# Kernel tuning notes

Measured on AMD Instinct MI355X. Metric: run time of the kernel, lower is better.

Reference implementation:

```python
import jax, jax.numpy as jnp
from jax import lax
import numpy as np
import math

B, LBL, PRED, CIN = 16, 48, 336, 7
L = LBL + PRED
DM, E = 512, 2
DIN, N, DCONV = 2 * DM, 16, 4
DTR = math.ceil(DM / 16)  # 32
TF = 4  # freq='h' time features
EPS = 1e-5


def _ln(x, w, b):
    m = x.mean(-1, keepdims=True)
    v = ((x - m) ** 2).mean(-1, keepdims=True)
    return (x - m) / jnp.sqrt(v + EPS) * w + b


def _silu(x):
    return x * jax.nn.sigmoid(x)


def _token_embed(x, w):
    # Conv1d(c_in, d_model, k=3, padding=1, circular, bias=False). x: (B,L,C), w: (DM,C,3)
    xp = jnp.concatenate([x[:, -1:], x, x[:, :1]], axis=1)  # circular pad along L
    y = lax.conv_general_dilated(xp.transpose(0, 2, 1), w, (1,), 'VALID',
                                 dimension_numbers=('NCH', 'OIH', 'NCH'))
    return y.transpose(0, 2, 1)  # (B,L,DM)


def _selective_scan(u, dt, A, Bm, Cm):
    # u,dt: (B,L,DIN); A: (DIN,N); Bm,Cm: (B,L,N)
    h0 = jnp.zeros((u.shape[0], DIN, N), u.dtype)

    def step(h, inp):
        u_t, dt_t, B_t, C_t = inp  # (B,DIN),(B,DIN),(B,N),(B,N)
        dA = jnp.exp(dt_t[:, :, None] * A)  # (B,DIN,N)
        h = dA * h + (dt_t * u_t)[:, :, None] * B_t[:, None, :]
        y = jnp.einsum('bdn,bn->bd', h, C_t)
        return h, y

    _, ys = lax.scan(step, h0, (u.transpose(1, 0, 2), dt.transpose(1, 0, 2),
                                Bm.transpose(1, 0, 2), Cm.transpose(1, 0, 2)))
    return ys.transpose(1, 0, 2)  # (B,L,DIN)


def _mamba(x, p):
    (in_w, conv_w, conv_b, xproj_w, dtproj_w, dtproj_b, A_log, Dp, out_w) = p
    xz = x @ in_w.T                      # (B,L,2*DIN)
    xin, z = jnp.split(xz, 2, axis=-1)
    # depthwise causal conv1d, kernel DCONV
    xt = jnp.pad(xin.transpose(0, 2, 1), ((0, 0), (0, 0), (DCONV - 1, 0)))
    xc = lax.conv_general_dilated(xt, conv_w, (1,), 'VALID', feature_group_count=DIN,
                                  dimension_numbers=('NCH', 'OIH', 'NCH'))
    xc = _silu((xc + conv_b[None, :, None]).transpose(0, 2, 1))  # (B,L,DIN)
    dbc = xc @ xproj_w.T                 # (B,L,DTR+2N)
    dt_r, Bm, Cm = dbc[..., :DTR], dbc[..., DTR:DTR + N], dbc[..., DTR + N:]
    dt = jax.nn.softplus(dt_r @ dtproj_w.T + dtproj_b)  # (B,L,DIN)
    A = -jnp.exp(A_log)                  # (DIN,N)
    y = _selective_scan(xc, dt, A, Bm, Cm) + xc * Dp
    y = y * _silu(z)
    return y @ out_w.T                   # (B,L,DM)


def _model(x_dec, x_mark_dec, token_w, timef_w, layer_ps, fin_w, fin_b, out_w):
    mean = lax.stop_gradient(x_dec[:, :LBL].mean(1, keepdims=True))
    head = x_dec[:, :LBL] - mean
    std = lax.stop_gradient(jnp.sqrt(head.var(axis=1, keepdims=True) + EPS))
    head = head / std
    xd = jnp.concatenate([head, x_dec[:, LBL:]], axis=1)
    x = _token_embed(xd, token_w) + x_mark_dec @ timef_w.T  # DataEmbedding_wo_pos (eval: no dropout)
    for i in range(E):
        nw, nb = layer_ps[0][i], layer_ps[1][i]
        mp = tuple(layer_ps[j][i] for j in range(2, 11))
        x = x + _mamba(_ln(x, nw, nb), mp)
    x = _ln(x, fin_w, fin_b)
    out = x @ out_w.T
    out = out * std + mean
    return out[:, -PRED:, :]


def setup_inputs() -> dict:
    key = jax.random.key(0)
    ks = jax.random.split(key, 20)
    s = 0.02
    d = {
        'x_enc': jax.random.normal(ks[0], (B, 96, CIN), jnp.float32),
        'x_mark_enc': jax.random.normal(ks[1], (B, 96, TF), jnp.float32),
        'x_dec': jax.random.normal(ks[2], (B, L, CIN), jnp.float32),
        'x_mark_dec': jax.random.normal(ks[3], (B, L, TF), jnp.float32),
        'token_w': jax.random.normal(ks[4], (DM, CIN, 3), jnp.float32) * s,
        'timef_w': jax.random.normal(ks[5], (DM, TF), jnp.float32) * s,
        'norm_w': jnp.ones((E, DM), jnp.float32),
        'norm_b': jnp.zeros((E, DM), jnp.float32),
        'in_proj_w': jax.random.normal(ks[6], (E, 2 * DIN, DM), jnp.float32) * s,
        'conv_w': jax.random.normal(ks[7], (E, DIN, 1, DCONV), jnp.float32) * s,
        'conv_b': jnp.zeros((E, DIN), jnp.float32),
        'xproj_w': jax.random.normal(ks[8], (E, DTR + 2 * N, DIN), jnp.float32) * s,
        'dtproj_w': jax.random.normal(ks[9], (E, DIN, DTR), jnp.float32) * s,
        'dtproj_b': jnp.full((E, DIN), -4.0, jnp.float32),
        'A_log': jnp.tile(jnp.log(jnp.arange(1, N + 1, dtype=jnp.float32)), (E, DIN, 1)),
        'D': jnp.ones((E, DIN), jnp.float32),
        'outproj_w': jax.random.normal(ks[10], (E, DM, DIN), jnp.float32) * s,
        'final_norm_w': jnp.ones((DM,), jnp.float32),
        'final_norm_b': jnp.zeros((DM,), jnp.float32),
        'out_w': jax.random.normal(ks[11], (CIN, DM), jnp.float32) * s,
    }
    return d


def reference(x_enc, x_mark_enc, x_dec, x_mark_dec, token_w, timef_w, norm_w, norm_b,
              in_proj_w, conv_w, conv_b, xproj_w, dtproj_w, dtproj_b, A_log, D,
              outproj_w, final_norm_w, final_norm_b, out_w):
    layer_ps = (norm_w, norm_b, in_proj_w, conv_w, conv_b, xproj_w, dtproj_w,
                dtproj_b, A_log, D, outproj_w)
    return _model(x_dec, x_mark_dec, token_w, timef_w, layer_ps,
                  final_norm_w, final_norm_b, out_w)
```

## Files before the change

kernel.cpp:

```cpp
#include <hip/hip_runtime.h>

#define B_    16
#define LBL_  48
#define PRED_ 336
#define CIN_  7
#define L_    384
#define DM_   512
#define E_    2
#define DIN_  1024
#define N_    16
#define DCONV_ 4
#define DTR_  32
#define TF_   4
#define EPSF  1e-5f
#define NSEG  16
#define SEGL  24
#define SC2   2
#define NCHK  12

typedef unsigned short u16;
typedef __attribute__((ext_vector_type(8))) short short8;
typedef __attribute__((ext_vector_type(4))) float f32x4;

__device__ __forceinline__ float bf2f(u16 u){
  union { float f; unsigned int i; } cv; cv.i = ((unsigned int)u) << 16; return cv.f;
}
__device__ __forceinline__ u16 f2bf(float f){
  union { float f; unsigned int i; } cv; cv.f = f;
  unsigned int x = cv.i;
  unsigned int lsb = (x >> 16) & 1u;
  x += 0x7fffu + lsb;
  return (u16)(x >> 16);
}
__device__ __forceinline__ float lo16(unsigned int v){
  union { float f; unsigned int i; } cv; cv.i = v << 16; return cv.f;
}
__device__ __forceinline__ float hi16(unsigned int v){
  union { float f; unsigned int i; } cv; cv.i = v & 0xffff0000u; return cv.f;
}

#define GLDS(g, l) __builtin_amdgcn_global_load_lds( \
    (const __attribute__((address_space(1))) void*)(g), \
    (__attribute__((address_space(3))) void*)(l), 16, 0, 0)

#define PO_XDEC   0
#define PO_XMARK  43008
#define PO_TOKW   67584
#define PO_TIMEF  78336
#define PO_NORMW  80384
#define PO_NORMB  81408
#define PO_INW    82432
#define PO_CONVW  2179584
#define PO_CONVB  2187776
#define PO_XPROJ  2189824
#define PO_DTW    2320896
#define PO_DTB    2386432
#define PO_ALOG   2388480
#define PO_DP     2421248
#define PO_OUTW   2423296
#define PO_FNW    3471872
#define PO_FNB    3472384
#define PO_HEADW  3472896
#define P_TOTAL   3476480
#define A_X    3476480
#define A_LNB  6622208
#define A_XZ   9767936
#define A_DT   22350848
#define A_DBC  28642304
#define A_MEAN 29078528
#define A_STD  29078640
#define A_DBC4 16059392
#define DBC_SL ((size_t)(B_*L_)*64)
#define A_XCB_OFF 3145728

struct Ptrs { const void* p[18]; };

__device__ __forceinline__ float wredsum(float s){
  #pragma unroll
  for (int off = 32; off; off >>= 1) s += __shfl_xor(s, off, 64);
  return s;
}

__device__ __forceinline__ void qpowers(float q, float* p){
  float q2 = q*q;
  float q4 = q2*q2;
  float q8 = q4*q4;
  float q3 = q2*q;
  p[0]=q;      p[1]=q2;     p[2]=q3;     p[3]=q4;
  p[4]=q4*q;   p[5]=q4*q2;  p[6]=q4*q3;  p[7]=q8;
  p[8]=q8*q;   p[9]=q8*q2;  p[10]=q8*q3; p[11]=q8*q4;
  p[12]=q8*p[4]; p[13]=q8*p[5]; p[14]=q8*p[6]; p[15]=q8*q8;
}

__device__ __forceinline__ unsigned int xcd_swz(unsigned int bid, unsigned int nwg){
  return (bid & 7u) * (nwg >> 3) + (bid >> 3);
}

__global__ __launch_bounds__(256) void convert_kernel(Ptrs ps, float* __restrict__ dst){
  const int offs[18] = {PO_XDEC, PO_XMARK, PO_TOKW, PO_TIMEF, PO_NORMW, PO_NORMB,
                        PO_INW, PO_CONVW, PO_CONVB, PO_XPROJ, PO_DTW, PO_DTB,
                        PO_ALOG, PO_DP, PO_OUTW, PO_FNW, PO_FNB, PO_HEADW};
  int idx = blockIdx.x * 256 + threadIdx.x;
  if (idx >= P_TOTAL) return;
  int seg = 0;
  #pragma unroll
  for (int s = 1; s < 18; s++) if (idx >= offs[s]) seg = s;
  int off = idx - offs[seg];
  int isbf = (((const u16*)ps.p[4])[0] == 0x3F80u);
  if (seg == 6 || seg == 9 || seg == 10 || seg == 14){
    u16 hv = isbf ? ((const u16*)ps.p[seg])[off]
                  : f2bf(((const float*)ps.p[seg])[off]);
    ((u16*)(dst + offs[seg]))[off] = hv;
  } else {
    float v = isbf ? bf2f(((const u16*)ps.p[seg])[off])
                   : ((const float*)ps.p[seg])[off];
    dst[idx] = v;
  }
}

__global__ __launch_bounds__(256) void embed_ln_kernel(const float* __restrict__ x_dec,
      const float* __restrict__ token_w, const float* __restrict__ x_mark,
      const float* __restrict__ timef_w, const float* __restrict__ nw,
      const float* __restrict__ nb, float* __restrict__ x, u16* __restrict__ out,
      float* __restrict__ meanv, float* __restrict__ stdv){
  __shared__ float sm[8], siv[8], ssd[8];
  int wv = threadIdx.x >> 6;
  int lane = threadIdx.x & 63;
  int tok = blockIdx.x*4 + wv;
  int t = tok % L_;
  int b = tok / L_;
  for (int c = wv; c < CIN_; c += 4){
    float v0 = (lane < LBL_) ? x_dec[(b*L_+lane)*CIN_+c] : 0.f;
    float m = wredsum(v0) * (1.f/LBL_);
    float dv = (lane < LBL_) ? (v0 - m) : 0.f;
    float sd = sqrtf(wredsum(dv*dv) * (1.f/LBL_) + EPSF);
    if (lane == 0){ sm[c] = m; siv[c] = 1.f/sd; ssd[c] = sd; }
  }
  __syncthreads();
  if ((blockIdx.x % (L_/4)) == 0 && threadIdx.x < CIN_){
    meanv[b*CIN_ + threadIdx.x] = sm[threadIdx.x];
    stdv[b*CIN_ + threadIdx.x]  = ssd[threadIdx.x];
  }
  int tm1 = (t == 0) ? L_-1 : t-1;
  int tp1 = (t == L_-1) ? 0 : t+1;
  auto ldx = [&](int row, int c){
    float v = x_dec[(b*L_+row)*CIN_+c];
    return (row < LBL_) ? (v - sm[c]) * siv[c] : v;
  };
  const float* mk = x_mark + (b*L_+t)*TF_;
  float a0[CIN_], a1[CIN_], a2[CIN_], mkv[TF_];
  #pragma unroll
  for (int ci = 0; ci < CIN_; ci++){ a0[ci]=ldx(tm1,ci); a1[ci]=ldx(t,ci); a2[ci]=ldx(tp1,ci); }
  #pragma unroll
  for (int f = 0; f < TF_; f++) mkv[f] = mk[f];
  float v[8];
  #pragma unroll
  for (int j = 0; j < 8; j++){
    int d = lane*8 + j;
    float acc = 0.f;
    #pragma unroll
    for (int ci = 0; ci < CIN_; ci++){
      const float* w = token_w + (d*CIN_+ci)*3;
      acc += a0[ci]*w[0] + a1[ci]*w[1] + a2[ci]*w[2];
    }
    #pragma unroll
    for (int f = 0; f < TF_; f++)
      acc += mkv[f] * timef_w[d*TF_+f];
    v[j] = acc;
  }
  float* xr = x + (size_t)tok*DM_ + lane*8;
  *(float4*)xr       = (float4){v[0],v[1],v[2],v[3]};
  *(float4*)(xr + 4) = (float4){v[4],v[5],v[6],v[7]};
  float s = (v[0]+v[1])+(v[2]+v[3])+((v[4]+v[5])+(v[6]+v[7]));
  float mean = wredsum(s) * (1.f/DM_);
  float s2 = 0.f;
  #pragma unroll
  for (int j = 0; j < 8; j++){ v[j] -= mean; s2 += v[j]*v[j]; }
  float rstd = rsqrtf(wredsum(s2) * (1.f/DM_) + EPSF);
  const float* wr = nw + lane*8;
  const float* br = nb + lane*8;
  uint4 o; unsigned int* op = (unsigned int*)&o;
  #pragma unroll
  for (int k = 0; k < 4; k++){
    u16 e0 = f2bf(v[2*k]   * rstd * wr[2*k]   + br[2*k]);
    u16 e1 = f2bf(v[2*k+1] * rstd * wr[2*k+1] + br[2*k+1]);
    op[k] = (unsigned int)e0 | ((unsigned int)e1 << 16);
  }
  *(uint4*)(out + (size_t)tok*DM_ + lane*8) = o;
}

__global__ __launch_bounds__(256) void ln_kernel(const float* __restrict__ x,
     const float* __restrict__ w, const float* __restrict__ bias, u16* __restrict__ out){
  int tok = blockIdx.x*4 + (threadIdx.x >> 6);
  int lane = threadIdx.x & 63;
  const float* xr = x + (size_t)tok*DM_ + lane*8;
  float4 a = *(const float4*)xr;
  float4 bq = *(const float4*)(xr + 4);
  float v[8] = {a.x,a.y,a.z,a.w,bq.x,bq.y,bq.z,bq.w};
  float s = (v[0]+v[1])+(v[2]+v[3])+((v[4]+v[5])+(v[6]+v[7]));
  float mean = wredsum(s) * (1.f/DM_);
  float s2 = 0.f;
  #pragma unroll
  for (int j = 0; j < 8; j++){ v[j] -= mean; s2 += v[j]*v[j]; }
  float rstd = rsqrtf(wredsum(s2) * (1.f/DM_) + EPSF);
  const float* wr = w + lane*8;
  const float* br = bias + lane*8;
  uint4 o; unsigned int* op = (unsigned int*)&o;
  #pragma unroll
  for (int k = 0; k < 4; k++){
    u16 e0 = f2bf(v[2*k]   * rstd * wr[2*k]   + br[2*k]);
    u16 e1 = f2bf(v[2*k+1] * rstd * wr[2*k+1] + br[2*k+1]);
    op[k] = (unsigned int)e0 | ((unsigned int)e1 << 16);
  }
  *(uint4*)(out + (size_t)tok*DM_ + lane*8) = o;
}

__global__ __launch_bounds__(256) void inproj_conv(const u16* __restrict__ A,
    const u16* __restrict__ Wt, const float* __restrict__ cw, const float* __restrict__ cb,
    u16* __restrict__ xz, u16* __restrict__ xcb){
  __shared__ u16 As[384 * 64];
  __shared__ u16 Ws[64 * 64];
  int tid = threadIdx.x;
  int wv = tid >> 6, lane = tid & 63;
  unsigned int bid = blockIdx.y * 32 + blockIdx.x;
  unsigned int swz = xcd_swz(bid, 512);
  int b  = (int)(swz >> 5);
  int n0 = (int)(swz & 31) * 64;
  int m0 = b * L_;
  int la = lane & 15, lk = lane >> 4;
  f32x4 acc[6][4];
  #pragma unroll
  for (int i = 0; i < 6; i++)
    #pragma unroll
    for (int j = 0; j < 4; j++) acc[i][j] = (f32x4){0.f,0.f,0.f,0.f};
  int sr = lane >> 3;
  int sc = (((lane & 7) ^ (sr & 7)) * 8);
  const u16* Ag = A + (size_t)(m0 + wv*96 + sr) * DM_ + sc;
  u16* Al = As + (wv*96)*64 + lane*8;
  const u16* Wg = Wt + (size_t)(n0 + wv*16 + sr) * DM_ + sc;
  u16* Wl = Ws + (wv*16)*64 + lane*8;
  for (int k0 = 0; k0 < DM_; k0 += 64){
    #pragma unroll
    for (int i = 0; i < 12; i++) GLDS(Ag + (size_t)(i*8)*DM_ + k0, Al + i*512);
    #pragma unroll
    for (int i = 0; i < 2; i++)  GLDS(Wg + (size_t)(i*8)*DM_ + k0, Wl + i*512);
    __syncthreads();
    #pragma unroll
    for (int ks = 0; ks < 2; ks++){
      int ch = (ks*4 + lk) ^ (la & 7);
      short8 af[6], bfr[4];
      #pragma unroll
      for (int mi = 0; mi < 6; mi++) af[mi] = *(const short8*)&As[(wv*96 + mi*16 + la)*64 + ch*8];
      #pragma unroll
      for (int ni = 0; ni < 4; ni++) bfr[ni] = *(const short8*)&Ws[(ni*16 + la)*64 + ch*8];
      #pragma unroll
      for (int mi = 0; mi < 6; mi++)
        #pragma unroll
        for (int ni = 0; ni < 4; ni++)
          acc[mi][ni] = __builtin_amdgcn_mfma_f32_16x16x32_bf16(af[mi], bfr[ni], acc[mi][ni], 0, 0, 0);
    }
    __syncthreads();
  }
  #pragma unroll
  for (int mi = 0; mi < 6; mi++)
    #pragma unroll
    for (int ni = 0; ni < 4; ni++){
      int colc = ni*2 + (la >> 3);
      #pragma unroll
      for (int r = 0; r < 4; r++){
        int row = wv*96 + mi*16 + lk*4 + r;
        As[row*64 + ((colc ^ (row & 7))<<3) + (la & 7)] = f2bf(acc[mi][ni][r]);
      }
    }
  __syncthreads();
  int c8 = (tid & 7) * 8;
  int tg = tid >> 3;
  if (n0 < DIN_){
    float4 w[8]; float bias[8];
    #pragma unroll
    for (int k = 0; k < 8; k++){
      w[k] = *(const float4*)(cw + (n0 + c8 + k)*4);
      bias[k] = cb[n0 + c8 + k];
    }
    for (int i = 0; i < 12; i++){
      int t = tg*12 + i;
      uint4 tap[4];
      #pragma unroll
      for (int j = 0; j < 4; j++){
        int rr = t - 3 + j;
        if (rr >= 0)
          tap[j] = *(const uint4*)&As[rr*64 + ((((c8>>3) ^ (rr & 7)))<<3)];
      }
      float v[8];
      #pragma unroll
      for (int k = 0; k < 8; k++){
        float s = bias[k];
        #pragma unroll
        for (int j = 0; j < 4; j++){
          if (j >= 3 - t){
            const unsigned int* tp = (const unsigned int*)&tap[j];
            float xv = (k & 1) ? hi16(tp[k >> 1]) : lo16(tp[k >> 1]);
            s += xv * ((const float*)&w[k])[j];
          }
        }
        v[k] = s / (1.f + __expf(-s));
      }
      uint4 o; unsigned int* op = (unsigned int*)&o;
      #pragma unroll
      for (int k = 0; k < 4; k++)
        op[k] = (unsigned int)f2bf(v[2*k]) | ((unsigned int)f2bf(v[2*k+1]) << 16);
      *(uint4*)(xcb + (size_t)(m0 + t)*DIN_ + n0 + c8) = o;
    }
  } else {
    for (int i = 0; i < 12; i++){
      int t = tg*12 + i;
      uint4 vq = *(const uint4*)&As[t*64 + ((((c8>>3) ^ (t & 7)))<<3)];
      *(uint4*)(xz + (size_t)(m0 + t)*(2*DIN_) + n0 + c8) = vq;
    }
  }
}

template<int TN, int ACCUM, int BF16OUT>
__global__ __launch_bounds__(256) void gemm_mfma(const u16* __restrict__ A, const u16* __restrict__ Wt,
    void* __restrict__ C, int M, int N, int K){
  constexpr int WN = TN / 2;
  constexpr int NI = WN / 16;
  __shared__ u16 As[128 * 64];
  __shared__ u16 Ws[TN * 64];
  int tid = threadIdx.x;
  int wv = tid >> 6, lane = tid & 63;
  int wm = (wv & 1) * 64, wn = (wv >> 1) * WN;
  unsigned int gx = gridDim.x;
  unsigned int bid = blockIdx.y * gx + blockIdx.x;
  unsigned int swz = xcd_swz(bid, gx * gridDim.y);
  int m0 = (int)(swz / gx) * 128, n0 = (int)(swz % gx) * TN;
  int la = lane & 15, lk = lane >> 4;
  f32x4 acc[4][NI];
  #pragma unroll
  for (int i = 0; i < 4; i++)
    #pragma unroll
    for (int j = 0; j < NI; j++) acc[i][j] = (f32x4){0.f, 0.f, 0.f, 0.f};
  int sr = lane >> 3;
  int sc = (((lane & 7) ^ (sr & 7)) * 8);
  const u16* Ag = A + (size_t)(m0 + wv*32 + sr) * K + sc;
  u16* Al = As + (wv*32)*64 + lane*8;
  const u16 *Wg; u16 *Wl;
  if constexpr (TN == 128){
    Wg = Wt + (size_t)(n0 + wv*32 + sr) * K + sc;
    Wl = Ws + (wv*32)*64 + lane*8;
  } else {
    Wg = Wt + (size_t)(n0 + wv*16 + sr) * K + sc;
    Wl = Ws + (wv*16)*64 + lane*8;
  }
  for (int k0 = 0; k0 < K; k0 += 64){
    #pragma unroll
    for (int i = 0; i < 4; i++) GLDS(Ag + (size_t)(i*8)*K + k0, Al + i*512);
    if constexpr (TN == 128){
      #pragma unroll
      for (int i = 0; i < 4; i++) GLDS(Wg + (size_t)(i*8)*K + k0, Wl + i*512);
    } else {
      #pragma unroll
      for (int i = 0; i < 2; i++) GLDS(Wg + (size_t)(i*8)*K + k0, Wl + i*512);
    }
    __syncthreads();
    #pragma unroll
    for (int ks = 0; ks < 2; ks++){
      short8 af[4], bfr[NI];
      int ch = (ks*4 + lk) ^ (la & 7);
      #pragma unroll
      for (int mi = 0; mi < 4; mi++) af[mi] = *(const short8*)&As[(wm + mi*16 + la)*64 + ch*8];
      #pragma unroll
      for (int ni = 0; ni < NI; ni++) bfr[ni] = *(const short8*)&Ws[(wn + ni*16 + la)*64 + ch*8];
      #pragma unroll
      for (int mi = 0; mi < 4; mi++)
        #pragma unroll
        for (int ni = 0; ni < NI; ni++)
          acc[mi][ni] = __builtin_amdgcn_mfma_f32_16x16x32_bf16(af[mi], bfr[ni], acc[mi][ni], 0, 0, 0);
    }
    __syncthreads();
  }
  #pragma unroll
  for (int mi = 0; mi < 4; mi++)
    #pragma unroll
    for (int ni = 0; ni < NI; ni++){
      int row = m0 + wm + mi*16 + lk*4;
      int col = n0 + wn + ni*16 + la;
      #pragma unroll
      for (int r = 0; r < 4; r++){
        if constexpr (BF16OUT){
          u16* p = (u16*)C + (size_t)row * N + col;
          p[(size_t)r * N] = f2bf(acc[mi][ni][r]);
        } else {
          float* p = (float*)C + (size_t)row * N + col;
          if (ACCUM) p[(size_t)r * N] += acc[mi][ni][r];
          else       p[(size_t)r * N]  = acc[mi][ni][r];
        }
      }
    }
}

__global__ __launch_bounds__(256) void xproj_mfma(const u16* __restrict__ A, const u16* __restrict__ Wt,
    float* __restrict__ out4){
  __shared__ u16 As[128 * 64];
  __shared__ u16 Ws[64 * 64];
  int tid = threadIdx.x;
  int wv = tid >> 6, lane = tid & 63;
  int wm = (wv & 1) * 64, wn = (wv >> 1) * 32;
  unsigned int gx = gridDim.x;
  unsigned int bid = blockIdx.y * gx + blockIdx.x;
  unsigned int swz = xcd_swz(bid, gx * gridDim.y);
  int m0 = (int)(swz / gx) * 128;
  int kc = (int)(swz % gx);
  int la = lane & 15, lk = lane >> 4;
  f32x4 acc[4][2];
  #pragma unroll
  for (int i = 0; i < 4; i++){ acc[i][0] = (f32x4){0.f,0.f,0.f,0.f}; acc[i][1] = (f32x4){0.f,0.f,0.f,0.f}; }
  int sr = lane >> 3;
  int sc = (((lane & 7) ^ (sr & 7)) * 8);
  const u16* Ag = A + (size_t)(m0 + wv*32 + sr) * DIN_ + kc*256 + sc;
  u16* Al = As + (wv*32)*64 + lane*8;
  const u16* Wg = Wt + (size_t)(wv*16 + sr) * DIN_ + kc*256 + sc;
  u16* Wl = Ws + (wv*16)*64 + lane*8;
  for (int k0 = 0; k0 < 256; k0 += 64){
    #pragma unroll
    for (int i = 0; i < 4; i++) GLDS(Ag + (size_t)(i*8)*DIN_ + k0, Al + i*512);
    #pragma unroll
    for (int i = 0; i < 2; i++) GLDS(Wg + (size_t)(i*8)*DIN_ + k0, Wl + i*512);
    __syncthreads();
    #pragma unroll
    for (int ks = 0; ks < 2; ks++){
      short8 af[4], bfr[2];
      int ch = (ks*4 + lk) ^ (la & 7);
      #pragma unroll
      for (int mi = 0; mi < 4; mi++) af[mi] = *(const short8*)&As[(wm + mi*16 + la)*64 + ch*8];
      #pragma unroll
      for (int ni = 0; ni < 2; ni++) bfr[ni] = *(const short8*)&Ws[(wn + ni*16 + la)*64 + ch*8];
      #pragma unroll
      for (int mi = 0; mi < 4; mi++)
        #pragma unroll
        for (int ni = 0; ni < 2; ni++)
          acc[mi][ni] = __builtin_amdgcn_mfma_f32_16x16x32_bf16(af[mi], bfr[ni], acc[mi][ni], 0, 0, 0);
    }
    __syncthreads();
  }
  #pragma unroll
  for (int mi = 0; mi < 4; mi++)
    #pragma unroll
    for (int ni = 0; ni < 2; ni++){
      int row = m0 + wm + mi*16 + lk*4;
      int col = wn + ni*16 + la;
      #pragma unroll
      for (int r = 0; r < 4; r++)
        out4[((size_t)kc*(B_*L_) + row + r)*64 + col] = acc[mi][ni][r];
    }
}

__global__ __launch_bounds__(256) void dtproj_mfma(const float* __restrict__ dbc4,
    const u16* __restrict__ dtwb, const float* __restrict__ dtb, u16* __restrict__ dt){
  __shared__ u16 As[128 * 32];
  __shared__ u16 Ws[64 * 32];
  int tid = threadIdx.x;
  int wv = tid >> 6, lane = tid & 63;
  int wm = (wv & 1) * 64, wn = (wv >> 1) * 32;
  unsigned int gx = gridDim.x;
  unsigned int bid = blockIdx.y * gx + blockIdx.x;
  unsigned int swz = xcd_swz(bid, gx * gridDim.y);
  int m0 = (int)(swz / gx) * 128, n0 = (int)(swz % gx) * 64;
  int la = lane & 15, lk = lane >> 4;
  int srow = lane >> 2, scol = (lane & 3) * 8;
  #pragma unroll
  for (int i = 0; i < 8; i++){
    int idx = i*512 + tid*2;
    int row = idx >> 5, col = idx & 31;
    const float* p = dbc4 + (size_t)(m0 + row)*64 + col;
    float s0 = 0.f, s1 = 0.f;
    #pragma unroll
    for (int k = 0; k < 4; k++){
      s0 += p[(size_t)k*DBC_SL];
      s1 += p[(size_t)k*DBC_SL + 1];
    }
    *(unsigned int*)&As[row*32 + col] = (unsigned int)f2bf(s0) | ((unsigned int)f2bf(s1) << 16);
  }
  GLDS(dtwb + (size_t)(n0 + wv*16 + srow)*32 + scol, Ws + wv*512 + lane*8);
  __syncthreads();
  short8 af[4], bfr[2];
  #pragma unroll
  for (int mi = 0; mi < 4; mi++) af[mi] = *(const short8*)&As[(wm + mi*16 + la)*32 + lk*8];
  #pragma unroll
  for (int ni = 0; ni < 2; ni++) bfr[ni] = *(const short8*)&Ws[(wn + ni*16 + la)*32 + lk*8];
  #pragma unroll
  for (int mi = 0; mi < 4; mi++)
    #pragma unroll
    for (int ni = 0; ni < 2; ni++){
      f32x4 acc = (f32x4){0.f,0.f,0.f,0.f};
      acc = __builtin_amdgcn_mfma_f32_16x16x32_bf16(af[mi], bfr[ni], acc, 0, 0, 0);
      int row = m0 + wm + mi*16 + lk*4;
      int d   = n0 + wn + ni*16 + la;
      float bias = dtb[d];
      #pragma unroll
      for (int r = 0; r < 4; r++){
        float raw = acc[r] + bias;
        float sp = (raw > 20.f) ? raw : log1pf(__expf(raw));
        dt[(size_t)(row + r)*DIN_ + d] = f2bf(sp);
      }
    }
}

#define WSTR2 896
__global__ __launch_bounds__(1024, 1) void scan_kernel(
    u16* __restrict__ ub_yb,
    const float* __restrict__ dbc, const u16* __restrict__ xz,
    const u16* __restrict__ dtp,
    const float* __restrict__ A_log, const float* __restrict__ Dp){
  __shared__ float smem[16384];

  int tid = threadIdx.x;
  int lane = tid & 63;
  int seg  = tid >> 6;
  int b = blockIdx.x >> 4;
  int g = blockIdx.x & 15;
  int d = g*64 + lane;
  size_t base = (size_t)b * L_;

  float* wbase = smem + seg * WSTR2;
  float* sbc = wbase;
  float* su  = wbase + 128;
  float* sz  = wbase + 384;
  float* sdt = wbase + 640;

  int st = lane >> 5;
  int j  = lane & 31;

  float A[16];
  #pragma unroll
  for (int n = 0; n < 16; n += 4){
    float4 av = *(const float4*)(A_log + (size_t)d*N_ + n);
    A[n] = -__expf(av.x); A[n+1] = -__expf(av.y); A[n+2] = -__expf(av.z); A[n+3] = -__expf(av.w);
  }
  float Dv = Dp[d];
  bool fastA = true;
  #pragma unroll
  for (int n = 0; n < 16; n++) fastA = fastA && (fabsf(A[n] + (float)(n+1)) < 1e-3f*(n+1));

  float h[16];
  #pragma unroll
  for (int n = 0; n < 16; n++) h[n] = 0.f;

  auto ldc = [&](int c, float& kbc, unsigned int& ku, unsigned int& kz,
                 unsigned int& kt, bool wz){
    size_t tokr = base + seg*SEGL + c*SC2 + st;
    const float* pb = dbc + tokr*64 + 32 + j;
    kbc = (pb[0] + pb[DBC_SL]) + (pb[2*DBC_SL] + pb[3*DBC_SL]);
    ku  = ((const unsigned int*)(ub_yb + tokr*DIN_ + g*64))[j];
    kt  = ((const unsigned int*)(dtp + tokr*DIN_ + g*64))[j];
    if (wz) kz = ((const unsigned int*)(xz + tokr*(2*DIN_) + DIN_ + g*64))[j];
  };
  auto stc = [&](int buf, float kbc, unsigned int ku, unsigned int kz,
                 unsigned int kt, bool wz){
    sbc[buf*64 + st*32 + j] = kbc;
    su [buf*128 + st*64 + 2*j]     = lo16(ku);
    su [buf*128 + st*64 + 2*j + 1] = hi16(ku);
    sdt[buf*128 + st*64 + 2*j]     = lo16(kt);
    sdt[buf*128 + st*64 + 2*j + 1] = hi16(kt);
    if (wz){
      sz[buf*128 + st*64 + 2*j]     = lo16(kz);
      sz[buf*128 + st*64 + 2*j + 1] = hi16(kz);
    }
  };

  float S = 0.f;
  {
    float kbc; unsigned int ku, kz, kt;
    ldc(0, kbc, ku, kz, kt, false);
    stc(0, kbc, ku, kz, kt, false);
    for (int c = 0; c < NCHK; c++){
      int cur = c & 1;
      bool have = (c + 1 < NCHK);
      float nbc; unsigned int nu, nz, nt;
      if (have) ldc(c+1, nbc, nu, nz, nt, false);
      for (int s = 0; s < SC2; s++){
        float dtv = sdt[cur*128 + s*64 + lane];
        float u   = su [cur*128 + s*64 + lane];
        const float* bcrow = sbc + cur*64 + s*32;
        float Bf[16];
        #pragma unroll
        for (int i = 0; i < 16; i += 4){
          float4 bv = *(const float4*)(bcrow + i);
          Bf[i] = bv.x; Bf[i+1] = bv.y; Bf[i+2] = bv.z; Bf[i+3] = bv.w;
        }
        float du = dtv * u;
        S += dtv;
        if (fastA){
          float q = __expf(-dtv);
          float p[16];
          qpowers(q, p);
          #pragma unroll
          for (int n = 0; n < 16; n++) h[n] = p[n] * h[n] + du * Bf[n];
        } else {
          #pragma unroll
          for (int n = 0; n < 16; n++){
            float dA = __expf(dtv * A[n]);
            h[n] = dA * h[n] + du * Bf[n];
          }
        }
      }
      if (have) stc(1 - cur, nbc, nu, nz, nt, false);
    }
  }

  #pragma unroll
  for (int half = 0; half < 2; half++){
    __syncthreads();
    #pragma unroll
    for (int n = 0; n < 8; n++){
      int nn = half*8 + n;
      smem[(n*NSEG + seg)*64 + lane]        = h[nn];
      smem[8192 + (n*NSEG + seg)*64 + lane] = __expf(A[nn] * S);
    }
    __syncthreads();
    float hs[8];
    #pragma unroll
    for (int n = 0; n < 8; n++) hs[n] = 0.f;
    for (int jj = 0; jj < seg; jj++){
      #pragma unroll
      for (int n = 0; n < 8; n++){
        float qh = smem[(n*NSEG + jj)*64 + lane];
        float qP = smem[8192 + (n*NSEG + jj)*64 + lane];
        hs[n] = qh + qP * hs[n];
      }
    }
    #pragma unroll
    for (int n = 0; n < 8; n++) h[half*8 + n] = hs[n];
  }
  __syncthreads();

  {
    float kbc; unsigned int ku, kz, kt;
    ldc(0, kbc, ku, kz, kt, true);
    stc(0, kbc, ku, kz, kt, true);
    for (int c = 0; c < NCHK; c++){
      int cur = c & 1;
      bool have = (c + 1 < NCHK);
      float nbc; unsigned int nu, nz, nt;
      if (have) ldc(c+1, nbc, nu, nz, nt, true);
      for (int s = 0; s < SC2; s++){
        float dtv = sdt[cur*128 + s*64 + lane];
        float u   = su [cur*128 + s*64 + lane];
        float z   = sz [cur*128 + s*64 + lane];
        const float* bcrow = sbc + cur*64 + s*32;
        float Bf[16], Cf[16];
        #pragma unroll
        for (int i = 0; i < 16; i += 4){
          float4 bv = *(const float4*)(bcrow + i);
          float4 cv = *(const float4*)(bcrow + 16 + i);
          Bf[i] = bv.x; Bf[i+1] = bv.y; Bf[i+2] = bv.z; Bf[i+3] = bv.w;
          Cf[i] = cv.x; Cf[i+1] = cv.y; Cf[i+2] = cv.z; Cf[i+3] = cv.w;
        }
        float du = dtv * u;
        float acc = 0.f;
        if (fastA){
          float q = __expf(-dtv);
          float p[16];
          qpowers(q, p);
          #pragma unroll
          for (int n = 0; n < 16; n++){
            h[n] = p[n] * h[n] + du * Bf[n];
            acc += h[n] * Cf[n];
          }
        } else {
          #pragma unroll
          for (int n = 0; n < 16; n++){
            float dA = __expf(dtv * A[n]);
            h[n] = dA * h[n] + du * Bf[n];
            acc += h[n] * Cf[n];
          }
        }
        float y = acc + u * Dv;
        size_t tok = base + seg*SEGL + c*SC2 + s;
        ub_yb[tok*DIN_ + d] = f2bf(y * (z / (1.f + __expf(-z))));
      }
      if (have) stc(1 - cur, nbc, nu, nz, nt, true);
    }
  }
}

__global__ __launch_bounds__(256) void head_kernel(const float* __restrict__ x,
    const float* __restrict__ fw, const float* __restrict__ fb, const float* __restrict__ ow,
    const float* __restrict__ meanv, const float* __restrict__ stdv, void* __restrict__ out,
    const u16* __restrict__ dtype_probe){
  int wav = blockIdx.x*4 + (threadIdx.x >> 6);
  int lane = threadIdx.x & 63;
  if (wav >= B_*PRED_) return;
  int b = wav / PRED_;
  int tt = wav % PRED_;
  int tok = b*L_ + LBL_ + tt;
  const float* xr = x + (size_t)tok*DM_ + lane*8;
  float4 a = *(const float4*)xr;
  float4 bq = *(const float4*)(xr + 4);
  float v[8] = {a.x,a.y,a.z,a.w,bq.x,bq.y,bq.z,bq.w};
  float s = (v[0]+v[1])+(v[2]+v[3])+((v[4]+v[5])+(v[6]+v[7]));
  float mean = wredsum(s) * (1.f/DM_);
  float s2 = 0.f;
  #pragma unroll
  for (int j = 0; j < 8; j++){ v[j] -= mean; s2 += v[j]*v[j]; }
  float rstd = rsqrtf(wredsum(s2) * (1.f/DM_) + EPSF);
  const float* fwr = fw + lane*8;
  const float* fbr = fb + lane*8;
  #pragma unroll
  for (int j = 0; j < 8; j++) v[j] = v[j] * rstd * fwr[j] + fbr[j];
  int isbf = (dtype_probe[0] == 0x3F80u);
  for (int o = 0; o < CIN_; o++){
    const float* owr = ow + (size_t)o*DM_ + lane*8;
    float part = 0.f;
    #pragma unroll
    for (int j = 0; j < 8; j++) part += v[j] * owr[j];
    part = wredsum(part);
    if (lane == 0){
      float res = part * stdv[b*CIN_ + o] + meanv[b*CIN_ + o];
      size_t oidx = (size_t)(b*PRED_ + tt)*CIN_ + o;
      if (isbf) ((u16*)out)[oidx] = f2bf(res);
      else      ((float*)out)[oidx] = res;
    }
  }
}

extern "C" void kernel_launch(void* const* d_in, const int* in_sizes, int n_in,
                              void* d_out, int out_size, void* d_ws, size_t ws_size,
                              hipStream_t stream){
  float* P = (float*)d_ws;

  Ptrs ps;
  for (int i = 0; i < 18; i++) ps.p[i] = d_in[2 + i];

  float* x    = P + A_X;
  u16*   lnxb = (u16*)(P + A_LNB);
  u16*   xz   = (u16*)(P + A_XZ);
  u16*   dt   = (u16*)(P + A_DT);
  u16*   xcb  = (u16*)(P + A_DT + A_XCB_OFF);
  float* dbc4 = P + A_DBC4;
  float* meanv= P + A_MEAN;
  float* stdv = P + A_STD;
  const u16* bwi = (const u16*)(P + PO_INW);
  const u16* bwx = (const u16*)(P + PO_XPROJ);
  const u16* bwd = (const u16*)(P + PO_DTW);
  const u16* bwo = (const u16*)(P + PO_OUTW);

  convert_kernel<<<(P_TOTAL+255)/256, 256, 0, stream>>>(ps, P);
  embed_ln_kernel<<<(B_*L_)/4, 256, 0, stream>>>(
      P + PO_XDEC, P + PO_TOKW, P + PO_XMARK, P + PO_TIMEF,
      P + PO_NORMW, P + PO_NORMB, x, lnxb, meanv, stdv);

  for (int e = 0; e < E_; e++){
    if (e > 0)
      ln_kernel<<<(B_*L_)/4, 256, 0, stream>>>(x, P + PO_NORMW + e*DM_, P + PO_NORMB + e*DM_, lnxb);
    inproj_conv<<<dim3(32, 16), 256, 0, stream>>>(
        lnxb, bwi + (size_t)e*2*DIN_*DM_,
        P + PO_CONVW + e*DIN_*DCONV_, P + PO_CONVB + e*DIN_, xz, xcb);
    xproj_mfma<<<dim3(4, (B_*L_)/128), 256, 0, stream>>>(
        xcb, bwx + (size_t)e*64*DIN_, dbc4);
    dtproj_mfma<<<dim3(DIN_/64, (B_*L_)/128), 256, 0, stream>>>(
        dbc4, bwd + (size_t)e*DIN_*DTR_, P + PO_DTB + e*DIN_, dt);
    scan_kernel<<<256, 1024, 0, stream>>>(
        xcb, dbc4, xz, dt, P + PO_ALOG + e*DIN_*N_, P + PO_DP + e*DIN_);
    gemm_mfma<64,1,0><<<dim3(DM_/64, (B_*L_)/128), 256, 0, stream>>>(
        xcb, bwo + (size_t)e*DM_*DIN_, x, B_*L_, DM_, DIN_);
  }

  head_kernel<<<(B_*PRED_+3)/4, 256, 0, stream>>>(
      x, P + PO_FNW, P + PO_FNB, P + PO_HEADW, meanv, stdv, d_out, (const u16*)d_in[6]);
}
```

Measured before the change: 392.8 us.

## Fuse dt projection and softplus into the selective scan kernel

Removes the separate dt-projection MFMA kernel and computes dt inside the scan: each lane holds its 32 dt-projection weights in registers and does a dot product with the dt_r slice of dbc staged in LDS, then applies softplus. This eliminates one kernel launch per layer and the write and read of the bf16 dt tensor. In exchange the serial scan loop gains a 32-term dot product and a transcendental per step, in both scan passes, and holds more registers.

```diff
diff --git a/kernel.cpp b/kernel.cpp
--- a/kernel.cpp
+++ b/kernel.cpp
@@ -66,7 +66,6 @@
 #define A_LNB  6622208
 #define A_XZ   9767936
 #define A_DT   22350848
-#define A_DBC  28642304
 #define A_MEAN 29078528
 #define A_STD  29078640
 #define A_DBC4 16059392
@@ -455,62 +454,11 @@
     }
 }
 
-__global__ __launch_bounds__(256) void dtproj_mfma(const float* __restrict__ dbc4,
-    const u16* __restrict__ dtwb, const float* __restrict__ dtb, u16* __restrict__ dt){
-  __shared__ u16 As[128 * 32];
-  __shared__ u16 Ws[64 * 32];
-  int tid = threadIdx.x;
-  int wv = tid >> 6, lane = tid & 63;
-  int wm = (wv & 1) * 64, wn = (wv >> 1) * 32;
-  unsigned int gx = gridDim.x;
-  unsigned int bid = blockIdx.y * gx + blockIdx.x;
-  unsigned int swz = xcd_swz(bid, gx * gridDim.y);
-  int m0 = (int)(swz / gx) * 128, n0 = (int)(swz % gx) * 64;
-  int la = lane & 15, lk = lane >> 4;
-  int srow = lane >> 2, scol = (lane & 3) * 8;
-  #pragma unroll
-  for (int i = 0; i < 8; i++){
-    int idx = i*512 + tid*2;
-    int row = idx >> 5, col = idx & 31;
-    const float* p = dbc4 + (size_t)(m0 + row)*64 + col;
-    float s0 = 0.f, s1 = 0.f;
-    #pragma unroll
-    for (int k = 0; k < 4; k++){
-      s0 += p[(size_t)k*DBC_SL];
-      s1 += p[(size_t)k*DBC_SL + 1];
-    }
-    *(unsigned int*)&As[row*32 + col] = (unsigned int)f2bf(s0) | ((unsigned int)f2bf(s1) << 16);
-  }
-  GLDS(dtwb + (size_t)(n0 + wv*16 + srow)*32 + scol, Ws + wv*512 + lane*8);
-  __syncthreads();
-  short8 af[4], bfr[2];
-  #pragma unroll
-  for (int mi = 0; mi < 4; mi++) af[mi] = *(const short8*)&As[(wm + mi*16 + la)*32 + lk*8];
-  #pragma unroll
-  for (int ni = 0; ni < 2; ni++) bfr[ni] = *(const short8*)&Ws[(wn + ni*16 + la)*32 + lk*8];
-  #pragma unroll
-  for (int mi = 0; mi < 4; mi++)
-    #pragma unroll
-    for (int ni = 0; ni < 2; ni++){
-      f32x4 acc = (f32x4){0.f,0.f,0.f,0.f};
-      acc = __builtin_amdgcn_mfma_f32_16x16x32_bf16(af[mi], bfr[ni], acc, 0, 0, 0);
-      int row = m0 + wm + mi*16 + lk*4;
-      int d   = n0 + wn + ni*16 + la;
-      float bias = dtb[d];
-      #pragma unroll
-      for (int r = 0; r < 4; r++){
-        float raw = acc[r] + bias;
-        float sp = (raw > 20.f) ? raw : log1pf(__expf(raw));
-        dt[(size_t)(row + r)*DIN_ + d] = f2bf(sp);
-      }
-    }
-}
-
-#define WSTR2 896
+#define WSTR2 768
 __global__ __launch_bounds__(1024, 1) void scan_kernel(
     u16* __restrict__ ub_yb,
     const float* __restrict__ dbc, const u16* __restrict__ xz,
-    const u16* __restrict__ dtp,
+    const u16* __restrict__ dtwb, const float* __restrict__ dtb,
     const float* __restrict__ A_log, const float* __restrict__ Dp){
   __shared__ float smem[16384];
 
@@ -524,9 +472,8 @@
 
   float* wbase = smem + seg * WSTR2;
   float* sbc = wbase;
-  float* su  = wbase + 128;
-  float* sz  = wbase + 384;
-  float* sdt = wbase + 640;
+  float* su  = wbase + 256;
+  float* sz  = wbase + 512;
 
   int st = lane >> 5;
   int j  = lane & 31;
@@ -538,6 +485,13 @@
     A[n] = -__expf(av.x); A[n+1] = -__expf(av.y); A[n+2] = -__expf(av.z); A[n+3] = -__expf(av.w);
   }
   float Dv = Dp[d];
+  unsigned int dtw[16];
+  {
+    const unsigned int* dwp = (const unsigned int*)(dtwb + (size_t)d*DTR_);
+    #pragma unroll
+    for (int i = 0; i < 16; i++) dtw[i] = dwp[i];
+  }
+  float dtbias = dtb[d];
   bool fastA = true;
   #pragma unroll
   for (int n = 0; n < 16; n++) fastA = fastA && (fabsf(A[n] + (float)(n+1)) < 1e-3f*(n+1));
@@ -546,42 +500,53 @@
   #pragma unroll
   for (int n = 0; n < 16; n++) h[n] = 0.f;
 
-  auto ldc = [&](int c, float& kbc, unsigned int& ku, unsigned int& kz,
-                 unsigned int& kt, bool wz){
+  auto ldc = [&](int c, float2& kbc, unsigned int& ku, unsigned int& kz, bool wz){
     size_t tokr = base + seg*SEGL + c*SC2 + st;
-    const float* pb = dbc + tokr*64 + 32 + j;
-    kbc = (pb[0] + pb[DBC_SL]) + (pb[2*DBC_SL] + pb[3*DBC_SL]);
+    const float* pb = dbc + tokr*64 + 2*j;
+    float2 v0 = *(const float2*)pb;
+    float2 v1 = *(const float2*)(pb + DBC_SL);
+    float2 v2 = *(const float2*)(pb + 2*DBC_SL);
+    float2 v3 = *(const float2*)(pb + 3*DBC_SL);
+    kbc.x = (v0.x + v1.x) + (v2.x + v3.x);
+    kbc.y = (v0.y + v1.y) + (v2.y + v3.y);
     ku  = ((const unsigned int*)(ub_yb + tokr*DIN_ + g*64))[j];
-    kt  = ((const unsigned int*)(dtp + tokr*DIN_ + g*64))[j];
     if (wz) kz = ((const unsigned int*)(xz + tokr*(2*DIN_) + DIN_ + g*64))[j];
   };
-  auto stc = [&](int buf, float kbc, unsigned int ku, unsigned int kz,
-                 unsigned int kt, bool wz){
-    sbc[buf*64 + st*32 + j] = kbc;
+  auto stc = [&](int buf, float2 kbc, unsigned int ku, unsigned int kz, bool wz){
+    sbc[buf*128 + st*64 + 2*j]     = kbc.x;
+    sbc[buf*128 + st*64 + 2*j + 1] = kbc.y;
     su [buf*128 + st*64 + 2*j]     = lo16(ku);
     su [buf*128 + st*64 + 2*j + 1] = hi16(ku);
-    sdt[buf*128 + st*64 + 2*j]     = lo16(kt);
-    sdt[buf*128 + st*64 + 2*j + 1] = hi16(kt);
     if (wz){
       sz[buf*128 + st*64 + 2*j]     = lo16(kz);
       sz[buf*128 + st*64 + 2*j + 1] = hi16(kz);
     }
   };
+  auto dtval = [&](const float* row){
+    float dacc = dtbias;
+    #pragma unroll
+    for (int i = 0; i < 16; i++){
+      unsigned int w2 = dtw[i];
+      dacc += row[2*i] * lo16(w2) + row[2*i+1] * hi16(w2);
+    }
+    return (dacc > 20.f) ? dacc : log1pf(__expf(dacc));
+  };
 
   float S = 0.f;
   {
-    float kbc; unsigned int ku, kz, kt;
-    ldc(0, kbc, ku, kz, kt, false);
-    stc(0, kbc, ku, kz, kt, false);
+    float2 kbc; unsigned int ku, kz;
+    ldc(0, kbc, ku, kz, false);
+    stc(0, kbc, ku, kz, false);
     for (int c = 0; c < NCHK; c++){
       int cur = c & 1;
       bool have = (c + 1 < NCHK);
-      float nbc; unsigned int nu, nz, nt;
-      if (have) ldc(c+1, nbc, nu, nz, nt, false);
+      float2 nbc; unsigned int nu, nz;
+      if (have) ldc(c+1, nbc, nu, nz, false);
       for (int s = 0; s < SC2; s++){
-        float dtv = sdt[cur*128 + s*64 + lane];
-        float u   = su [cur*128 + s*64 + lane];
-        const float* bcrow = sbc + cur*64 + s*32;
+        const float* row = sbc + cur*128 + s*64;
+        float dtv = dtval(row);
+        float u   = su[cur*128 + s*64 + lane];
+        const float* bcrow = row + 32;
         float Bf[16];
         #pragma unroll
         for (int i = 0; i < 16; i += 4){
@@ -604,7 +569,7 @@
           }
         }
       }
-      if (have) stc(1 - cur, nbc, nu, nz, nt, false);
+      if (have) stc(1 - cur, nbc, nu, nz, false);
     }
   }
 
@@ -635,19 +600,20 @@
   __syncthreads();
 
   {
-    float kbc; unsigned int ku, kz, kt;
-    ldc(0, kbc, ku, kz, kt, true);
-    stc(0, kbc, ku, kz, kt, true);
+    float2 kbc; unsigned int ku, kz;
+    ldc(0, kbc, ku, kz, true);
+    stc(0, kbc, ku, kz, true);
     for (int c = 0; c < NCHK; c++){
       int cur = c & 1;
       bool have = (c + 1 < NCHK);
-      float nbc; unsigned int nu, nz, nt;
-      if (have) ldc(c+1, nbc, nu, nz, nt, true);
+      float2 nbc; unsigned int nu, nz;
+      if (have) ldc(c+1, nbc, nu, nz, true);
       for (int s = 0; s < SC2; s++){
-        float dtv = sdt[cur*128 + s*64 + lane];
-        float u   = su [cur*128 + s*64 + lane];
-        float z   = sz [cur*128 + s*64 + lane];
-        const float* bcrow = sbc + cur*64 + s*32;
+        const float* row = sbc + cur*128 + s*64;
+        float dtv = dtval(row);
+        float u   = su[cur*128 + s*64 + lane];
+        float z   = sz[cur*128 + s*64 + lane];
+        const float* bcrow = row + 32;
         float Bf[16], Cf[16];
         #pragma unroll
         for (int i = 0; i < 16; i += 4){
@@ -679,7 +645,7 @@
         size_t tok = base + seg*SEGL + c*SC2 + s;
         ub_yb[tok*DIN_ + d] = f2bf(y * (z / (1.f + __expf(-z))));
       }
-      if (have) stc(1 - cur, nbc, nu, nz, nt, true);
+      if (have) stc(1 - cur, nbc, nu, nz, true);
     }
   }
 }
@@ -735,7 +701,6 @@
   float* x    = P + A_X;
   u16*   lnxb = (u16*)(P + A_LNB);
   u16*   xz   = (u16*)(P + A_XZ);
-  u16*   dt   = (u16*)(P + A_DT);
   u16*   xcb  = (u16*)(P + A_DT + A_XCB_OFF);
   float* dbc4 = P + A_DBC4;
   float* meanv= P + A_MEAN;
@@ -758,10 +723,9 @@
         P + PO_CONVW + e*DIN_*DCONV_, P + PO_CONVB + e*DIN_, xz, xcb);
     xproj_mfma<<<dim3(4, (B_*L_)/128), 256, 0, stream>>>(
         xcb, bwx + (size_t)e*64*DIN_, dbc4);
-    dtproj_mfma<<<dim3(DIN_/64, (B_*L_)/128), 256, 0, stream>>>(
-        dbc4, bwd + (size_t)e*DIN_*DTR_, P + PO_DTB + e*DIN_, dt);
     scan_kernel<<<256, 1024, 0, stream>>>(
-        xcb, dbc4, xz, dt, P + PO_ALOG + e*DIN_*N_, P + PO_DP + e*DIN_);
+        xcb, dbc4, xz, bwd + (size_t)e*DIN_*DTR_, P + PO_DTB + e*DIN_,
+        P + PO_ALOG + e*DIN_*N_, P + PO_DP + e*DIN_);
     gemm_mfma<64,1,0><<<dim3(DM_/64, (B_*L_)/128), 256, 0, stream>>>(
         xcb, bwo + (size_t)e*DM_*DIN_, x, B_*L_, DM_, DIN_);
   }
```

New measurement: 459.0 us. +16.9%, slower.

## Fuse x_proj and dt_proj into one kernel, dropping split-K partials

Applied to the files above, without the earlier changes.

Replaces the split-K x_proj kernel (four partial-sum slices) and the separate dt_proj kernel with a single kernel. Each block computes the full K=1024 reduction for 32 rows, keeps the result in shared memory, and immediately runs the dt projection plus softplus for all 1024 channels. It also writes a compact summed B/C buffer, so the scan reads one value instead of summing four partials. The cost is less parallelism: 192 blocks each run a serial K loop with no double buffering, where the old split-K kernel had more concurrency.

```diff
diff --git a/kernel.cpp b/kernel.cpp
--- a/kernel.cpp
+++ b/kernel.cpp
@@ -66,11 +66,9 @@
 #define A_LNB  6622208
 #define A_XZ   9767936
 #define A_DT   22350848
-#define A_DBC  28642304
+#define A_DBCS 28642304
 #define A_MEAN 29078528
 #define A_STD  29078640
-#define A_DBC4 16059392
-#define DBC_SL ((size_t)(B_*L_)*64)
 #define A_XCB_OFF 3145728
 
 struct Ptrs { const void* p[18]; };
@@ -399,117 +397,104 @@
     }
 }
 
-__global__ __launch_bounds__(256) void xproj_mfma(const u16* __restrict__ A, const u16* __restrict__ Wt,
-    float* __restrict__ out4){
-  __shared__ u16 As[128 * 64];
+__global__ __launch_bounds__(256) void xdt_mfma(const u16* __restrict__ A,
+    const u16* __restrict__ Wt, const u16* __restrict__ dtwb, const float* __restrict__ dtb,
+    u16* __restrict__ dt, float* __restrict__ dbcs){
+  __shared__ u16 As[32 * 64];
   __shared__ u16 Ws[64 * 64];
+  __shared__ float Ds[32 * 66];
+  __shared__ u16 Wd[64 * 32];
+  __shared__ u16 Db[32 * 72];
   int tid = threadIdx.x;
   int wv = tid >> 6, lane = tid & 63;
-  int wm = (wv & 1) * 64, wn = (wv >> 1) * 32;
-  unsigned int gx = gridDim.x;
-  unsigned int bid = blockIdx.y * gx + blockIdx.x;
-  unsigned int swz = xcd_swz(bid, gx * gridDim.y);
-  int m0 = (int)(swz / gx) * 128;
-  int kc = (int)(swz % gx);
+  unsigned int swz = xcd_swz(blockIdx.x, 192);
+  int m0 = (int)swz * 32;
   int la = lane & 15, lk = lane >> 4;
-  f32x4 acc[4][2];
-  #pragma unroll
-  for (int i = 0; i < 4; i++){ acc[i][0] = (f32x4){0.f,0.f,0.f,0.f}; acc[i][1] = (f32x4){0.f,0.f,0.f,0.f}; }
+  int wm = (wv & 1) * 16, wn = (wv >> 1) * 32;
+
+  f32x4 acc[2];
+  acc[0] = (f32x4){0.f,0.f,0.f,0.f};
+  acc[1] = (f32x4){0.f,0.f,0.f,0.f};
   int sr = lane >> 3;
   int sc = (((lane & 7) ^ (sr & 7)) * 8);
-  const u16* Ag = A + (size_t)(m0 + wv*32 + sr) * DIN_ + kc*256 + sc;
-  u16* Al = As + (wv*32)*64 + lane*8;
-  const u16* Wg = Wt + (size_t)(wv*16 + sr) * DIN_ + kc*256 + sc;
-  u16* Wl = Ws + (wv*16)*64 + lane*8;
-  for (int k0 = 0; k0 < 256; k0 += 64){
-    #pragma unroll
-    for (int i = 0; i < 4; i++) GLDS(Ag + (size_t)(i*8)*DIN_ + k0, Al + i*512);
-    #pragma unroll
-    for (int i = 0; i < 2; i++) GLDS(Wg + (size_t)(i*8)*DIN_ + k0, Wl + i*512);
+  const u16* Ag = A + (size_t)(m0 + wv*8 + sr) * DIN_ + sc;
+  u16* Al = As + (wv*8)*64 + lane*8;
+  const u16* Wg0 = Wt + (size_t)(wv*16 + sr) * DIN_ + sc;
+  const u16* Wg1 = Wt + (size_t)(wv*16 + 8 + sr) * DIN_ + sc;
+  u16* Wl0 = Ws + (wv*16)*64 + lane*8;
+  u16* Wl1 = Ws + (wv*16 + 8)*64 + lane*8;
+  for (int k0 = 0; k0 < DIN_; k0 += 64){
+    GLDS(Ag + k0, Al);
+    GLDS(Wg0 + k0, Wl0);
+    GLDS(Wg1 + k0, Wl1);
     __syncthreads();
     #pragma unroll
     for (int ks = 0; ks < 2; ks++){
-      short8 af[4], bfr[2];
       int ch = (ks*4 + lk) ^ (la & 7);
-      #pragma unroll
-      for (int mi = 0; mi < 4; mi++) af[mi] = *(const short8*)&As[(wm + mi*16 + la)*64 + ch*8];
-      #pragma unroll
-      for (int ni = 0; ni < 2; ni++) bfr[ni] = *(const short8*)&Ws[(wn + ni*16 + la)*64 + ch*8];
-      #pragma unroll
-      for (int mi = 0; mi < 4; mi++)
-        #pragma unroll
-        for (int ni = 0; ni < 2; ni++)
-          acc[mi][ni] = __builtin_amdgcn_mfma_f32_16x16x32_bf16(af[mi], bfr[ni], acc[mi][ni], 0, 0, 0);
-    }
-    __syncthreads();
-  }
-  #pragma unroll
-  for (int mi = 0; mi < 4; mi++)
+      short8 af = *(const short8*)&As[(wm + la)*64 + ch*8];
+      #pragma unroll
+      for (int ni = 0; ni < 2; ni++){
+        short8 bfr = *(const short8*)&Ws[(wn + ni*16 + la)*64 + ch*8];
+        acc[ni] = __builtin_amdgcn_mfma_f32_16x16x32_bf16(af, bfr, acc[ni], 0, 0, 0);
+      }
+    }
+    __syncthreads();
+  }
+  #pragma unroll
+  for (int ni = 0; ni < 2; ni++)
+    #pragma unroll
+    for (int r = 0; r < 4; r++)
+      Ds[(wm + lk*4 + r)*66 + wn + ni*16 + la] = acc[ni][r];
+  __syncthreads();
+  {
+    int row = tid >> 3;
+    int c4  = (tid & 7) * 4;
+    float4 v = {Ds[row*66 + 32 + c4], Ds[row*66 + 33 + c4],
+                Ds[row*66 + 34 + c4], Ds[row*66 + 35 + c4]};
+    *(float4*)&dbcs[(size_t)(m0 + row)*32 + c4] = v;
+  }
+  short8 af2;
+  {
+    u16 tmp[8];
+    #pragma unroll
+    for (int i = 0; i < 8; i++)
+      tmp[i] = f2bf(Ds[(wm + la)*66 + lk*8 + i]);
+    af2 = *(const short8*)tmp;
+  }
+
+  int srd = lane >> 2;
+  int scd = (((lane & 3) ^ (srd & 3)) * 8);
+  for (int nt = 0; nt < 16; nt++){
+    GLDS(dtwb + (size_t)(nt*64 + wv*16 + srd)*32 + scd, Wd + (wv*16)*32 + lane*8);
+    __syncthreads();
     #pragma unroll
     for (int ni = 0; ni < 2; ni++){
-      int row = m0 + wm + mi*16 + lk*4;
-      int col = wn + ni*16 + la;
-      #pragma unroll
-      for (int r = 0; r < 4; r++)
-        out4[((size_t)kc*(B_*L_) + row + r)*64 + col] = acc[mi][ni][r];
-    }
-}
-
-__global__ __launch_bounds__(256) void dtproj_mfma(const float* __restrict__ dbc4,
-    const u16* __restrict__ dtwb, const float* __restrict__ dtb, u16* __restrict__ dt){
-  __shared__ u16 As[128 * 32];
-  __shared__ u16 Ws[64 * 32];
-  int tid = threadIdx.x;
-  int wv = tid >> 6, lane = tid & 63;
-  int wm = (wv & 1) * 64, wn = (wv >> 1) * 32;
-  unsigned int gx = gridDim.x;
-  unsigned int bid = blockIdx.y * gx + blockIdx.x;
-  unsigned int swz = xcd_swz(bid, gx * gridDim.y);
-  int m0 = (int)(swz / gx) * 128, n0 = (int)(swz % gx) * 64;
-  int la = lane & 15, lk = lane >> 4;
-  int srow = lane >> 2, scol = (lane & 3) * 8;
-  #pragma unroll
-  for (int i = 0; i < 8; i++){
-    int idx = i*512 + tid*2;
-    int row = idx >> 5, col = idx & 31;
-    const float* p = dbc4 + (size_t)(m0 + row)*64 + col;
-    float s0 = 0.f, s1 = 0.f;
-    #pragma unroll
-    for (int k = 0; k < 4; k++){
-      s0 += p[(size_t)k*DBC_SL];
-      s1 += p[(size_t)k*DBC_SL + 1];
-    }
-    *(unsigned int*)&As[row*32 + col] = (unsigned int)f2bf(s0) | ((unsigned int)f2bf(s1) << 16);
-  }
-  GLDS(dtwb + (size_t)(n0 + wv*16 + srow)*32 + scol, Ws + wv*512 + lane*8);
-  __syncthreads();
-  short8 af[4], bfr[2];
-  #pragma unroll
-  for (int mi = 0; mi < 4; mi++) af[mi] = *(const short8*)&As[(wm + mi*16 + la)*32 + lk*8];
-  #pragma unroll
-  for (int ni = 0; ni < 2; ni++) bfr[ni] = *(const short8*)&Ws[(wn + ni*16 + la)*32 + lk*8];
-  #pragma unroll
-  for (int mi = 0; mi < 4; mi++)
-    #pragma unroll
-    for (int ni = 0; ni < 2; ni++){
-      f32x4 acc = (f32x4){0.f,0.f,0.f,0.f};
-      acc = __builtin_amdgcn_mfma_f32_16x16x32_bf16(af[mi], bfr[ni], acc, 0, 0, 0);
-      int row = m0 + wm + mi*16 + lk*4;
-      int d   = n0 + wn + ni*16 + la;
+      int rw = wn + ni*16 + la;
+      int ch2 = (lk ^ (la & 3)) * 8;
+      short8 bfr2 = *(const short8*)&Wd[rw*32 + ch2];
+      f32x4 a2 = (f32x4){0.f,0.f,0.f,0.f};
+      a2 = __builtin_amdgcn_mfma_f32_16x16x32_bf16(af2, bfr2, a2, 0, 0, 0);
+      int d = nt*64 + wn + ni*16 + la;
       float bias = dtb[d];
       #pragma unroll
       for (int r = 0; r < 4; r++){
-        float raw = acc[r] + bias;
-        float sp = (raw > 20.f) ? raw : log1pf(__expf(raw));
-        dt[(size_t)(row + r)*DIN_ + d] = f2bf(sp);
-      }
-    }
+        float raw = a2[r] + bias;
+        float sp = (raw > 20.f) ? raw : __logf(1.f + __expf(raw));
+        Db[(wm + lk*4 + r)*72 + wn + ni*16 + la] = f2bf(sp);
+      }
+    }
+    __syncthreads();
+    int row = tid >> 3;
+    int c8  = (tid & 7) * 8;
+    uint4 o = *(const uint4*)&Db[row*72 + c8];
+    *(uint4*)&dt[(size_t)(m0 + row)*DIN_ + nt*64 + c8] = o;
+  }
 }
 
 #define WSTR2 896
 __global__ __launch_bounds__(1024, 1) void scan_kernel(
     u16* __restrict__ ub_yb,
-    const float* __restrict__ dbc, const u16* __restrict__ xz,
+    const float* __restrict__ dbcs, const u16* __restrict__ xz,
     const u16* __restrict__ dtp,
     const float* __restrict__ A_log, const float* __restrict__ Dp){
   __shared__ float smem[16384];
@@ -549,8 +534,7 @@
   auto ldc = [&](int c, float& kbc, unsigned int& ku, unsigned int& kz,
                  unsigned int& kt, bool wz){
     size_t tokr = base + seg*SEGL + c*SC2 + st;
-    const float* pb = dbc + tokr*64 + 32 + j;
-    kbc = (pb[0] + pb[DBC_SL]) + (pb[2*DBC_SL] + pb[3*DBC_SL]);
+    kbc = dbcs[tokr*32 + j];
     ku  = ((const unsigned int*)(ub_yb + tokr*DIN_ + g*64))[j];
     kt  = ((const unsigned int*)(dtp + tokr*DIN_ + g*64))[j];
     if (wz) kz = ((const unsigned int*)(xz + tokr*(2*DIN_) + DIN_ + g*64))[j];
@@ -737,7 +721,7 @@
   u16*   xz   = (u16*)(P + A_XZ);
   u16*   dt   = (u16*)(P + A_DT);
   u16*   xcb  = (u16*)(P + A_DT + A_XCB_OFF);
-  float* dbc4 = P + A_DBC4;
+  float* dbcs = P + A_DBCS;
   float* meanv= P + A_MEAN;
   float* stdv = P + A_STD;
   const u16* bwi = (const u16*)(P + PO_INW);
@@ -756,12 +740,11 @@
     inproj_conv<<<dim3(32, 16), 256, 0, stream>>>(
         lnxb, bwi + (size_t)e*2*DIN_*DM_,
         P + PO_CONVW + e*DIN_*DCONV_, P + PO_CONVB + e*DIN_, xz, xcb);
-    xproj_mfma<<<dim3(4, (B_*L_)/128), 256, 0, stream>>>(
-        xcb, bwx + (size_t)e*64*DIN_, dbc4);
-    dtproj_mfma<<<dim3(DIN_/64, (B_*L_)/128), 256, 0, stream>>>(
-        dbc4, bwd + (size_t)e*DIN_*DTR_, P + PO_DTB + e*DIN_, dt);
+    xdt_mfma<<<192, 256, 0, stream>>>(
+        xcb, bwx + (size_t)e*64*DIN_, bwd + (size_t)e*DIN_*DTR_,
+        P + PO_DTB + e*DIN_, dt, dbcs);
     scan_kernel<<<256, 1024, 0, stream>>>(
-        xcb, dbc4, xz, dt, P + PO_ALOG + e*DIN_*N_, P + PO_DP + e*DIN_);
+        xcb, dbcs, xz, dt, P + PO_ALOG + e*DIN_*N_, P + PO_DP + e*DIN_);
     gemm_mfma<64,1,0><<<dim3(DM_/64, (B_*L_)/128), 256, 0, stream>>>(
         xcb, bwo + (size_t)e*DM_*DIN_, x, B_*L_, DM_, DIN_);
   }
```

Result: faster. 379.5 us (-3.4%).
